# Performance work log

Hardware: AMD Instinct MI355X
Metric: run time of the kernel (lower is better)

## Reference

```python
import jax, jax.numpy as jnp
import numpy as np

EMB = 128  # embedding_size hard-coded in source
NW = 8192  # weak samples
NS = 8192  # strong samples
FD = 1024  # encoder input feature dim
QN = 1024  # queue max_size
C = 80     # num classes (COCO-style WSOD)


def setup_inputs() -> dict:
    key = jax.random.key(0)
    ks = jax.random.split(key, 9)
    return {
        "feats_strong": jax.random.normal(ks[0], (NS, FD), jnp.float32),
        "feats_weak": jax.random.normal(ks[1], (NW, FD), jnp.float32),
        "strong_labels": jax.random.randint(ks[2], (NS,), 0, C, jnp.int64),
        "weak_labels": jax.random.randint(ks[3], (NW,), 0, C, jnp.int64),
        "Wq": jax.random.normal(ks[4], (FD, EMB), jnp.float32) * (FD ** -0.5),
        "bq": jax.random.normal(ks[5], (EMB,), jnp.float32) * 0.01,
        "Wk": jax.random.normal(ks[6], (FD, EMB), jnp.float32) * (FD ** -0.5),
        "bk": jax.random.normal(ks[7], (EMB,), jnp.float32) * 0.01,
        "queue": jax.random.normal(ks[8], (QN, EMB), jnp.float32),
    }


def reference(feats_strong, feats_weak, strong_labels, weak_labels, Wq, bq, Wk, bk, queue):
    # Encoders applied to all samples at once (original loops one-by-one).
    q_all = feats_weak @ Wq + bq            # [NW, EMB]
    k_all = feats_strong @ Wk + bk          # [NS, EMB]
    k_all = jax.lax.stop_gradient(k_all)    # k = k.detach() in source

    w, s = weak_labels, strong_labels
    eq_ws = w[:, None] == s[None, :]                      # [NW, NS] weak-vs-strong label match
    cnt = eq_ws.astype(jnp.int32).sum(1)                  # num_strong per weak sample
    valid = cnt > 0                                       # `if weak_label in strong_labels`

    # rank of i among weak indices with the same label (position in torch.where output)
    eq_ww = (w[:, None] == w[None, :]).astype(jnp.int32)
    rank = jnp.tril(eq_ww, -1).sum(1)                     # [NW]
    sel = rank % jnp.maximum(cnt, 1)                      # `% num_strong`

    # occurrence rank of each strong index within its label group
    eq_ss = (s[:, None] == s[None, :]).astype(jnp.int32)
    occ = jnp.tril(eq_ss, -1).sum(1)                      # [NS]

    # index_strong[i] = sel[i]-th strong index whose label == w[i]
    M = eq_ws & (occ[None, :] == sel[:, None])            # [NW, NS]
    idx = jnp.argmax(M, axis=1)                           # [NW]

    q = q_all                                             # [NW, EMB]
    k = k_all[idx]                                        # [NW, EMB]

    l_pos = jnp.sum(q * k, axis=-1, keepdims=True)        # bmm([N,1,E],[N,E,1]) -> [N,1]
    l_neg = q @ queue.reshape(EMB, -1)                    # queue.view(EMB, -1): row-major reshape
    logits = jnp.concatenate([l_pos, l_neg], axis=1)      # [NW, 1+QN]

    # CrossEntropy with target 0 on each valid row, mean over valid rows
    ce = -jax.nn.log_softmax(logits, axis=-1)[:, 0]
    m = valid.astype(logits.dtype)
    loss = jnp.sum(ce * m) / jnp.maximum(m.sum(), 1.0)
    return loss
```

## Files before the change

kernel.cpp:

```cpp
#include <hip/hip_runtime.h>
#include <hip/hip_bf16.h>

#define NW   8192
#define NS   8192
#define FD   1024
#define EMB  128
#define QN   1024
#define NC   80

typedef unsigned short ushort_t;
typedef unsigned int   uint_t;
typedef __attribute__((ext_vector_type(8))) short short8;
typedef __attribute__((ext_vector_type(4))) float f32x4;

#define OFF_Q      0u
#define OFF_K      1048576u
#define OFF_WTQ    2097152u
#define OFF_WTK    2129920u
#define OFF_HIST   2752512u
#define OFF_RANK   2752640u
#define OFF_CNT    2760832u
#define OFF_BHS    2785408u
#define OFF_BHW    2787968u
#define OFF_ACC    2790528u
#define OFF_QT     2790532u
#define OFF_TABLE  3000000u

__device__ __forceinline__ ushort_t f2bf(float f) {
    uint_t u = __float_as_uint(f);
    u = (u + 0x7fffu + ((u >> 16) & 1u)) >> 16;
    return (ushort_t)u;
}
__device__ __forceinline__ uint_t pack2(float a, float b) {
    return (uint_t)f2bf(a) | ((uint_t)f2bf(b) << 16);
}

#define GLOAD_LDS16(gp, lp)                                                     \
    __builtin_amdgcn_global_load_lds(                                           \
        (const __attribute__((address_space(1))) void*)(gp),                    \
        (__attribute__((address_space(3))) void*)(lp), 16, 0, 0)

__global__ __launch_bounds__(256) void cvtbh_k(const float* __restrict__ Wq,
                                               const float* __restrict__ Wk,
                                               const float* __restrict__ queue,
                                               const int* __restrict__ s_lab,
                                               const int* __restrict__ w_lab,
                                               ushort_t* __restrict__ Wtq,
                                               ushort_t* __restrict__ Wtk,
                                               ushort_t* __restrict__ Qt,
                                               int* __restrict__ bhs,
                                               int* __restrict__ bhw,
                                               float* __restrict__ accum,
                                               int* __restrict__ counter) {
    int bx = blockIdx.x;
    int t = threadIdx.x;
    if (bx >= 384) {
        __shared__ int h[NC];
        int b2 = bx - 384, z = b2 >> 5, cb = b2 & 31;
        const int* lab = z ? w_lab : s_lab;
        int* bh = z ? bhw : bhs;
        if (t < NC) h[t] = 0;
        __syncthreads();
        atomicAdd(&h[lab[cb * 256 + t]], 1);
        __syncthreads();
        if (t < NC) bh[cb * NC + t] = h[t];
        return;
    }
    __shared__ float tile[32][33];
    int z = bx >> 7, flat = bx & 127;
    if (z == 0 && flat == 0) {
        if (t < 2) accum[t] = 0.0f;
        if (t == 2) *counter = 0;
    }
    const float* in; ushort_t* out; int r0, c0, C;
    if (z < 2) { in = z ? Wk : Wq; out = z ? Wtk : Wtq; C = 128;
                 r0 = (flat >> 2) * 32; c0 = (flat & 3) * 32; }
    else       { in = queue; out = Qt; C = 1024;
                 r0 = (flat & 3) * 32; c0 = (flat >> 2) * 32; }
    int i = t >> 3, j0 = (t & 7) * 4;
    float4 v = *(const float4*)(in + (size_t)(r0 + i) * C + c0 + j0);
    tile[i][j0] = v.x; tile[i][j0 + 1] = v.y; tile[i][j0 + 2] = v.z; tile[i][j0 + 3] = v.w;
    __syncthreads();
    uint2 pk;
    pk.x = pack2(tile[j0][i], tile[j0 + 1][i]);
    pk.y = pack2(tile[j0 + 2][i], tile[j0 + 3][i]);
    size_t oaddr;
    if (z < 2) {
        int k0 = r0 + j0, n = c0 + i;
        oaddr = (size_t)(k0 >> 5) * 4096 + (size_t)((k0 >> 3) & 3) * 1024
              + (size_t)n * 8 + (k0 & 7);
    } else {
        oaddr = (size_t)(c0 + i) * 128 + (r0 + j0);
    }
    *(uint2*)(out + oaddr) = pk;
}

__global__ __launch_bounds__(256) void enc_mfma_k(const float* __restrict__ A0,
                                                  const float* __restrict__ A1,
                                                  const ushort_t* __restrict__ Wt0,
                                                  const ushort_t* __restrict__ Wt1,
                                                  const float* __restrict__ b0_,
                                                  const float* __restrict__ b1_,
                                                  float* __restrict__ out0,
                                                  float* __restrict__ out1,
                                                  const int* __restrict__ s_lab,
                                                  const int* __restrict__ w_lab,
                                                  const int* __restrict__ bhs,
                                                  const int* __restrict__ bhw,
                                                  int* __restrict__ table,
                                                  int* __restrict__ rank,
                                                  int* __restrict__ hist) {
    __shared__ __align__(16) char smem[20480];

    int bx = blockIdx.x;
    int t = threadIdx.x;

    if (bx >= 1024) {
        int* ll = (int*)smem;
        int b2 = bx - 1024, z = b2 >> 5, cb = b2 & 31;
        const int* lab = z ? w_lab : s_lab;
        const int* bh = z ? bhw : bhs;
        int j = cb * 256 + t;
        int c = lab[j];
        ll[t] = c;
        __syncthreads();
        int r = 0;
        for (int b = 0; b < cb; b++) r += bh[b * NC + c];
        for (int jj = 0; jj < t; jj++) r += (ll[jj] == c) ? 1 : 0;
        if (z) rank[j] = r;
        else   table[c * 8192 + r] = j;
        if (b2 == 0 && t < 128) {
            int h = 0;
            if (t < NC)
                for (int b = 0; b < 32; b++) h += bhs[b * NC + t];
            hist[t] = h;
        }
        return;
    }

    int which = bx >> 9;
    int mtile = bx & 511;
    const float*    A    = which ? A1 : A0;
    const ushort_t* Wt   = which ? Wt1 : Wt0;
    const float*    bias = which ? b1_ : b0_;
    float*          out  = which ? out1 : out0;
    int row0 = mtile * 16;

    int wv = t >> 6, ln = t & 63;
    int lane15 = ln & 15, kg = ln >> 4;

    const float* gA = A + (size_t)(row0 + wv * 8 + (ln >> 3)) * FD + ((ln & 7) ^ (ln >> 3)) * 4;
    const ushort_t* gB = Wt + (size_t)wv * 1024 + ln * 8;

    f32x4 acc0 = (f32x4){0.f, 0.f, 0.f, 0.f};
    f32x4 acc1 = (f32x4){0.f, 0.f, 0.f, 0.f};

#define STAGE(BUF, KB)                                                           \
    { char* lb = smem + (BUF) * 10240;                                           \
      if (wv < 2) GLOAD_LDS16(gA + (size_t)(KB) * 32, lb + wv * 1024);           \
      const ushort_t* gb = gB + (size_t)(KB) * 4096;                             \
      char* bb = lb + 2048 + wv * 2048;                                          \
      GLOAD_LDS16(gb,       bb);                                                 \
      GLOAD_LDS16(gb + 512, bb + 1024); }

    STAGE(0, 0)
    __syncthreads();

#pragma unroll 1
    for (int kb = 0; kb < 32; kb++) {
        int cur = kb & 1;
        if (kb < 31) STAGE(cur ^ 1, kb + 1)
        char* lb = smem + cur * 10240;
        float4 alo = *(const float4*)(lb + (lane15 * 8 + ((2 * kg)     ^ (lane15 & 7))) * 16);
        float4 ahi = *(const float4*)(lb + (lane15 * 8 + ((2 * kg + 1) ^ (lane15 & 7))) * 16);
        uint4 pk;
        pk.x = pack2(alo.x, alo.y); pk.y = pack2(alo.z, alo.w);
        pk.z = pack2(ahi.x, ahi.y); pk.w = pack2(ahi.z, ahi.w);
        short8 af = __builtin_bit_cast(short8, pk);
        uint4 bb0 = *(const uint4*)(lb + 2048 + ((size_t)kg * 128 + wv * 32 + lane15) * 16);
        uint4 bb1 = *(const uint4*)(lb + 2048 + ((size_t)kg * 128 + wv * 32 + 16 + lane15) * 16);
        acc0 = __builtin_amdgcn_mfma_f32_16x16x32_bf16(af, __builtin_bit_cast(short8, bb0), acc0, 0, 0, 0);
        acc1 = __builtin_amdgcn_mfma_f32_16x16x32_bf16(af, __builtin_bit_cast(short8, bb1), acc1, 0, 0, 0);
        __syncthreads();
    }
#undef STAGE

    {
        int col0 = wv * 32 + lane15, col1 = wv * 32 + 16 + lane15;
        float bv0 = bias[col0], bv1 = bias[col1];
        int rbase = row0 + kg * 4;
#pragma unroll
        for (int j = 0; j < 4; j++) {
            out[(size_t)(rbase + j) * EMB + col0] = acc0[j] + bv0;
            out[(size_t)(rbase + j) * EMB + col1] = acc1[j] + bv1;
        }
    }
}

__global__ __launch_bounds__(256, 2) void ce_mfma_k(const float* __restrict__ q,
                                                    const float* __restrict__ k,
                                                    const ushort_t* __restrict__ Qt,
                                                    const int* __restrict__ rank,
                                                    const int* __restrict__ table,
                                                    const int* __restrict__ w,
                                                    const int* __restrict__ hist,
                                                    float* __restrict__ accum,
                                                    int* __restrict__ counter,
                                                    float* __restrict__ outp) {
    __shared__ int   idx_lds[16];
    __shared__ float lpos_lds[16];
    __shared__ float mg[4][16][2];
    int t = threadIdx.x;
    int r0 = blockIdx.x * 16;

    if (t < 16) {
        int i = r0 + t;
        int c = w[i];
        int cc = hist[c];
        idx_lds[t] = (cc > 0) ? table[c * 8192 + (rank[i] % cc)] : 0;
    }
    __syncthreads();

    {
        int rr = t >> 4;
        int o = (t & 15) * 8;
        const float4* qa = (const float4*)(q + (size_t)(r0 + rr) * EMB + o);
        const float4* ka = (const float4*)(k + (size_t)idx_lds[rr] * EMB + o);
        float4 a0 = qa[0], b0 = ka[0], a1 = qa[1], b1 = ka[1];
        float s = a0.x * b0.x + a0.y * b0.y + a0.z * b0.z + a0.w * b0.w
                + a1.x * b1.x + a1.y * b1.y + a1.z * b1.z + a1.w * b1.w;
        s += __shfl_xor(s, 1); s += __shfl_xor(s, 2);
        s += __shfl_xor(s, 4); s += __shfl_xor(s, 8);
        if ((t & 15) == 0) lpos_lds[rr] = s;
    }

    int wv = t >> 6, ln = t & 63;
    int lane15 = ln & 15, kg = ln >> 4;

    short8 afr[4];
#pragma unroll
    for (int ks = 0; ks < 4; ks++) {
        const float4* p = (const float4*)(q + (size_t)(r0 + lane15) * EMB + ks * 32 + kg * 8);
        float4 a = p[0], b = p[1];
        uint4 pk;
        pk.x = pack2(a.x, a.y); pk.y = pack2(a.z, a.w);
        pk.z = pack2(b.x, b.y); pk.w = pack2(b.z, b.w);
        afr[ks] = __builtin_bit_cast(short8, pk);
    }

    f32x4 accA[8], accB[8];
#pragma unroll
    for (int nc = 0; nc < 8; nc++) {
        accA[nc] = (f32x4){0.f, 0.f, 0.f, 0.f};
        accB[nc] = (f32x4){0.f, 0.f, 0.f, 0.f};
    }
#pragma unroll
    for (int nc = 0; nc < 8; nc++) {
        size_t nrow0 = (size_t)(nc * 128 + wv * 32 + lane15) * 128 + kg * 8;
#pragma unroll
        for (int ks = 0; ks < 4; ks++) {
            short8 bf0 = __builtin_bit_cast(short8, *(const uint4*)(Qt + nrow0 + ks * 32));
            short8 bf1 = __builtin_bit_cast(short8, *(const uint4*)(Qt + nrow0 + 16 * 128 + ks * 32));
            accA[nc] = __builtin_amdgcn_mfma_f32_16x16x32_bf16(afr[ks], bf0, accA[nc], 0, 0, 0);
            accB[nc] = __builtin_amdgcn_mfma_f32_16x16x32_bf16(afr[ks], bf1, accB[nc], 0, 0, 0);
        }
    }

#pragma unroll
    for (int j = 0; j < 4; j++) {
        float mx = -1e30f;
#pragma unroll
        for (int nc = 0; nc < 8; nc++) mx = fmaxf(mx, fmaxf(accA[nc][j], accB[nc][j]));
        mx = fmaxf(mx, __shfl_xor(mx, 1));
        mx = fmaxf(mx, __shfl_xor(mx, 2));
        mx = fmaxf(mx, __shfl_xor(mx, 4));
        mx = fmaxf(mx, __shfl_xor(mx, 8));
        float s = 0.f;
#pragma unroll
        for (int nc = 0; nc < 8; nc++)
            s += __expf(accA[nc][j] - mx) + __expf(accB[nc][j] - mx);
        s += __shfl_xor(s, 1);
        s += __shfl_xor(s, 2);
        s += __shfl_xor(s, 4);
        s += __shfl_xor(s, 8);
        if (lane15 == 0) {
            mg[wv][kg * 4 + j][0] = mx;
            mg[wv][kg * 4 + j][1] = s;
        }
    }
    __syncthreads();
    if (wv == 0) {
        float cv = 0.f, cc = 0.f;
        if (t < 16) {
            int i = r0 + t;
            float m0 = mg[0][t][0], l0 = mg[0][t][1];
            float m1 = mg[1][t][0], l1 = mg[1][t][1];
            float m2 = mg[2][t][0], l2 = mg[2][t][1];
            float m3 = mg[3][t][0], l3 = mg[3][t][1];
            float lp = lpos_lds[t];
            float m = fmaxf(fmaxf(fmaxf(m0, m1), fmaxf(m2, m3)), lp);
            float l = l0 * __expf(m0 - m) + l1 * __expf(m1 - m)
                    + l2 * __expf(m2 - m) + l3 * __expf(m3 - m) + __expf(lp - m);
            float ce = -(lp - m - __logf(l));
            if (hist[w[i]] > 0) { cv = ce; cc = 1.f; }
        }
        cv += __shfl_xor(cv, 1);  cc += __shfl_xor(cc, 1);
        cv += __shfl_xor(cv, 2);  cc += __shfl_xor(cc, 2);
        cv += __shfl_xor(cv, 4);  cc += __shfl_xor(cc, 4);
        cv += __shfl_xor(cv, 8);  cc += __shfl_xor(cc, 8);
        if (t == 0) {
            atomicAdd(&accum[0], cv);
            atomicAdd(&accum[1], cc);
            __threadfence();
            int done = atomicAdd(counter, 1);
            if (done == 511) {
                float s = atomicAdd(&accum[0], 0.0f);
                float c = atomicAdd(&accum[1], 0.0f);
                outp[0] = s / fmaxf(c, 1.0f);
            }
        }
    }
}

extern "C" void kernel_launch(void* const* d_in, const int* in_sizes, int n_in,
                              void* d_out, int out_size, void* d_ws, size_t ws_size,
                              hipStream_t stream) {
    const float* feats_strong = (const float*)d_in[0];
    const float* feats_weak   = (const float*)d_in[1];
    const int*   s_lab        = (const int*)d_in[2];
    const int*   w_lab        = (const int*)d_in[3];
    const float* Wq           = (const float*)d_in[4];
    const float* bq           = (const float*)d_in[5];
    const float* Wk           = (const float*)d_in[6];
    const float* bk           = (const float*)d_in[7];
    const float* queue        = (const float*)d_in[8];

    float*    wsf = (float*)d_ws;
    int*      wsi = (int*)d_ws;

    float*    q_g   = wsf + OFF_Q;
    float*    k_g   = wsf + OFF_K;
    int*      table = wsi + OFF_TABLE;
    ushort_t* Wtq   = (ushort_t*)(wsi + OFF_WTQ);
    ushort_t* Wtk   = (ushort_t*)(wsi + OFF_WTK);
    int*      hist  = wsi + OFF_HIST;
    int*      rank  = wsi + OFF_RANK;
    int*      cnt   = wsi + OFF_CNT;
    int*      bhs   = wsi + OFF_BHS;
    int*      bhw   = wsi + OFF_BHW;
    float*    accum = wsf + OFF_ACC;
    ushort_t* Qt    = (ushort_t*)(wsi + OFF_QT);

    cvtbh_k<<<448, 256, 0, stream>>>(Wq, Wk, queue, s_lab, w_lab,
                                     Wtq, Wtk, Qt, bhs, bhw, accum, cnt);
    enc_mfma_k<<<1088, 256, 0, stream>>>(feats_weak, feats_strong, Wtq, Wtk, bq, bk, q_g, k_g,
                                         s_lab, w_lab, bhs, bhw, table, rank, hist);
    ce_mfma_k<<<512, 256, 0, stream>>>(q_g, k_g, Qt, rank, table, w_lab, hist,
                                       accum, cnt, (float*)d_out);
}
```

Before: 170.2 us.

## Enlarge encoder GEMM tiles and stage queue through swizzled LDS in CE kernel

The encoder GEMM now computes 32-row tiles with a 2x2 wave layout over a 64-wide K step, so each wave issues four MFMAs per A fragment. This halves the grid and the number of K iterations, and raises reuse of B per byte loaded. The weight pre-layout changes to match the 64-wide K blocking. In the CE kernel, the transposed queue is laid out with an XOR swizzle and streamed through double-buffered LDS via global-to-LDS loads, replacing direct global fragment reads. The trade-off is more LDS per block (48KB encoder, 32KB CE), which may lower occupancy, plus an extra barrier per N chunk in the CE loop.

```diff
diff --git a/kernel.cpp b/kernel.cpp
--- a/kernel.cpp
+++ b/kernel.cpp
@@ -85,12 +85,13 @@
     pk.x = pack2(tile[j0][i], tile[j0 + 1][i]);
     pk.y = pack2(tile[j0 + 2][i], tile[j0 + 3][i]);
     size_t oaddr;
+    int k0 = r0 + j0, n = c0 + i;
     if (z < 2) {
-        int k0 = r0 + j0, n = c0 + i;
-        oaddr = (size_t)(k0 >> 5) * 4096 + (size_t)((k0 >> 3) & 3) * 1024
+        oaddr = (size_t)(k0 >> 6) * 8192 + (size_t)((k0 >> 3) & 7) * 1024
               + (size_t)n * 8 + (k0 & 7);
     } else {
-        oaddr = (size_t)(c0 + i) * 128 + (r0 + j0);
+        int c = k0 >> 3;
+        oaddr = ((size_t)n * 16 + (c ^ (n & 15))) * 8 + (k0 & 7);
     }
     *(uint2*)(out + oaddr) = pk;
 }
@@ -110,14 +111,14 @@
                                                   int* __restrict__ table,
                                                   int* __restrict__ rank,
                                                   int* __restrict__ hist) {
-    __shared__ __align__(16) char smem[20480];
+    __shared__ __align__(16) char smem[49152];
 
     int bx = blockIdx.x;
     int t = threadIdx.x;
 
-    if (bx >= 1024) {
+    if (bx >= 512) {
         int* ll = (int*)smem;
-        int b2 = bx - 1024, z = b2 >> 5, cb = b2 & 31;
+        int b2 = bx - 512, z = b2 >> 5, cb = b2 & 31;
         const int* lab = z ? w_lab : s_lab;
         const int* bh = z ? bhw : bhs;
         int j = cb * 256 + t;
@@ -138,62 +139,78 @@
         return;
     }
 
-    int which = bx >> 9;
-    int mtile = bx & 511;
+    int which = bx >> 8;
+    int mtile = bx & 255;
     const float*    A    = which ? A1 : A0;
     const ushort_t* Wt   = which ? Wt1 : Wt0;
     const float*    bias = which ? b1_ : b0_;
     float*          out  = which ? out1 : out0;
-    int row0 = mtile * 16;
+    int row0 = mtile * 32;
 
     int wv = t >> 6, ln = t & 63;
+    int wm = wv >> 1, wn = wv & 1;
     int lane15 = ln & 15, kg = ln >> 4;
 
-    const float* gA = A + (size_t)(row0 + wv * 8 + (ln >> 3)) * FD + ((ln & 7) ^ (ln >> 3)) * 4;
-    const ushort_t* gB = Wt + (size_t)wv * 1024 + ln * 8;
-
-    f32x4 acc0 = (f32x4){0.f, 0.f, 0.f, 0.f};
-    f32x4 acc1 = (f32x4){0.f, 0.f, 0.f, 0.f};
+    int ar0 = wv * 8 + (ln >> 4);
+    int ar1 = ar0 + 4;
+    const float* gA0 = A + (size_t)(row0 + ar0) * FD + (((ln & 15) ^ (ar0 & 15))) * 4;
+    const float* gA1 = A + (size_t)(row0 + ar1) * FD + (((ln & 15) ^ (ar1 & 15))) * 4;
+    const ushort_t* gB = Wt + (size_t)wv * 2048 + ln * 8;
+
+    f32x4 acc[4];
+#pragma unroll
+    for (int nt = 0; nt < 4; nt++) acc[nt] = (f32x4){0.f, 0.f, 0.f, 0.f};
 
 #define STAGE(BUF, KB)                                                           \
-    { char* lb = smem + (BUF) * 10240;                                           \
-      if (wv < 2) GLOAD_LDS16(gA + (size_t)(KB) * 32, lb + wv * 1024);           \
-      const ushort_t* gb = gB + (size_t)(KB) * 4096;                             \
-      char* bb = lb + 2048 + wv * 2048;                                          \
-      GLOAD_LDS16(gb,       bb);                                                 \
-      GLOAD_LDS16(gb + 512, bb + 1024); }
+    { char* lb = smem + (BUF) * 24576;                                           \
+      GLOAD_LDS16(gA0 + (size_t)(KB) * 64, lb + wv * 2048);                      \
+      GLOAD_LDS16(gA1 + (size_t)(KB) * 64, lb + wv * 2048 + 1024);               \
+      const ushort_t* gb = gB + (size_t)(KB) * 8192;                             \
+      char* bb = lb + 8192 + wv * 4096;                                          \
+      GLOAD_LDS16(gb,        bb);                                                \
+      GLOAD_LDS16(gb + 512,  bb + 1024);                                         \
+      GLOAD_LDS16(gb + 1024, bb + 2048);                                         \
+      GLOAD_LDS16(gb + 1536, bb + 3072); }
 
     STAGE(0, 0)
     __syncthreads();
 
 #pragma unroll 1
-    for (int kb = 0; kb < 32; kb++) {
+    for (int kb = 0; kb < 16; kb++) {
         int cur = kb & 1;
-        if (kb < 31) STAGE(cur ^ 1, kb + 1)
-        char* lb = smem + cur * 10240;
-        float4 alo = *(const float4*)(lb + (lane15 * 8 + ((2 * kg)     ^ (lane15 & 7))) * 16);
-        float4 ahi = *(const float4*)(lb + (lane15 * 8 + ((2 * kg + 1) ^ (lane15 & 7))) * 16);
-        uint4 pk;
-        pk.x = pack2(alo.x, alo.y); pk.y = pack2(alo.z, alo.w);
-        pk.z = pack2(ahi.x, ahi.y); pk.w = pack2(ahi.z, ahi.w);
-        short8 af = __builtin_bit_cast(short8, pk);
-        uint4 bb0 = *(const uint4*)(lb + 2048 + ((size_t)kg * 128 + wv * 32 + lane15) * 16);
-        uint4 bb1 = *(const uint4*)(lb + 2048 + ((size_t)kg * 128 + wv * 32 + 16 + lane15) * 16);
-        acc0 = __builtin_amdgcn_mfma_f32_16x16x32_bf16(af, __builtin_bit_cast(short8, bb0), acc0, 0, 0, 0);
-        acc1 = __builtin_amdgcn_mfma_f32_16x16x32_bf16(af, __builtin_bit_cast(short8, bb1), acc1, 0, 0, 0);
+        if (kb < 15) STAGE(cur ^ 1, kb + 1)
+        char* lb = smem + cur * 24576;
+#pragma unroll
+        for (int ks = 0; ks < 2; ks++) {
+            int r_l = wm * 16 + lane15;
+            int c0 = ks * 8 + kg * 2;
+            float4 alo = *(const float4*)(lb + ((size_t)r_l * 16 + ((c0)     ^ (r_l & 15))) * 16);
+            float4 ahi = *(const float4*)(lb + ((size_t)r_l * 16 + ((c0 + 1) ^ (r_l & 15))) * 16);
+            uint4 pk;
+            pk.x = pack2(alo.x, alo.y); pk.y = pack2(alo.z, alo.w);
+            pk.z = pack2(ahi.x, ahi.y); pk.w = pack2(ahi.z, ahi.w);
+            short8 af = __builtin_bit_cast(short8, pk);
+            int kgg = ks * 4 + kg;
+#pragma unroll
+            for (int nt = 0; nt < 4; nt++) {
+                uint4 bb = *(const uint4*)(lb + 8192 +
+                            ((size_t)kgg * 128 + wn * 64 + nt * 16 + lane15) * 16);
+                acc[nt] = __builtin_amdgcn_mfma_f32_16x16x32_bf16(
+                    af, __builtin_bit_cast(short8, bb), acc[nt], 0, 0, 0);
+            }
+        }
         __syncthreads();
     }
 #undef STAGE
 
-    {
-        int col0 = wv * 32 + lane15, col1 = wv * 32 + 16 + lane15;
-        float bv0 = bias[col0], bv1 = bias[col1];
-        int rbase = row0 + kg * 4;
-#pragma unroll
-        for (int j = 0; j < 4; j++) {
-            out[(size_t)(rbase + j) * EMB + col0] = acc0[j] + bv0;
-            out[(size_t)(rbase + j) * EMB + col1] = acc1[j] + bv1;
-        }
+#pragma unroll
+    for (int nt = 0; nt < 4; nt++) {
+        int col = wn * 64 + nt * 16 + lane15;
+        float bv = bias[col];
+        int rbase = row0 + wm * 16 + kg * 4;
+#pragma unroll
+        for (int j = 0; j < 4; j++)
+            out[(size_t)(rbase + j) * EMB + col] = acc[nt][j] + bv;
     }
 }
 
@@ -207,6 +224,7 @@
                                                     float* __restrict__ accum,
                                                     int* __restrict__ counter,
                                                     float* __restrict__ outp) {
+    __shared__ __align__(16) char bsm[32768];
     __shared__ int   idx_lds[16];
     __shared__ float lpos_lds[16];
     __shared__ float mg[4][16][2];
@@ -248,37 +266,51 @@
         afr[ks] = __builtin_bit_cast(short8, pk);
     }
 
-    f32x4 accA[8], accB[8];
-#pragma unroll
-    for (int nc = 0; nc < 8; nc++) {
-        accA[nc] = (f32x4){0.f, 0.f, 0.f, 0.f};
-        accB[nc] = (f32x4){0.f, 0.f, 0.f, 0.f};
-    }
-#pragma unroll
-    for (int nc = 0; nc < 8; nc++) {
-        size_t nrow0 = (size_t)(nc * 128 + wv * 32 + lane15) * 128 + kg * 8;
+    f32x4 acc[16];
+#pragma unroll
+    for (int nc = 0; nc < 16; nc++) acc[nc] = (f32x4){0.f, 0.f, 0.f, 0.f};
+
+#define STAGE_CE(BUF, NC)                                                        \
+    { char* lb = bsm + (BUF) * 16384;                                            \
+      const ushort_t* src = Qt + (size_t)(NC) * 8192 + wv * 2048 + ln * 8;       \
+      char* bb = lb + wv * 4096;                                                 \
+      GLOAD_LDS16(src,        bb);                                               \
+      GLOAD_LDS16(src + 512,  bb + 1024);                                        \
+      GLOAD_LDS16(src + 1024, bb + 2048);                                        \
+      GLOAD_LDS16(src + 1536, bb + 3072); }
+
+    STAGE_CE(0, 0)
+    __syncthreads();
+
+#pragma unroll
+    for (int nc = 0; nc < 16; nc++) {
+        int cur = nc & 1;
+        if (nc < 15) STAGE_CE(cur ^ 1, nc + 1)
+        char* lb = bsm + cur * 16384;
+        int n_l = wv * 16 + lane15;
 #pragma unroll
         for (int ks = 0; ks < 4; ks++) {
-            short8 bf0 = __builtin_bit_cast(short8, *(const uint4*)(Qt + nrow0 + ks * 32));
-            short8 bf1 = __builtin_bit_cast(short8, *(const uint4*)(Qt + nrow0 + 16 * 128 + ks * 32));
-            accA[nc] = __builtin_amdgcn_mfma_f32_16x16x32_bf16(afr[ks], bf0, accA[nc], 0, 0, 0);
-            accB[nc] = __builtin_amdgcn_mfma_f32_16x16x32_bf16(afr[ks], bf1, accB[nc], 0, 0, 0);
-        }
-    }
+            int c = ks * 4 + kg;
+            uint4 bb = *(const uint4*)(lb + ((size_t)n_l * 16 + (c ^ lane15)) * 16);
+            acc[nc] = __builtin_amdgcn_mfma_f32_16x16x32_bf16(
+                afr[ks], __builtin_bit_cast(short8, bb), acc[nc], 0, 0, 0);
+        }
+        __syncthreads();
+    }
+#undef STAGE_CE
 
 #pragma unroll
     for (int j = 0; j < 4; j++) {
         float mx = -1e30f;
 #pragma unroll
-        for (int nc = 0; nc < 8; nc++) mx = fmaxf(mx, fmaxf(accA[nc][j], accB[nc][j]));
+        for (int nc = 0; nc < 16; nc++) mx = fmaxf(mx, acc[nc][j]);
         mx = fmaxf(mx, __shfl_xor(mx, 1));
         mx = fmaxf(mx, __shfl_xor(mx, 2));
         mx = fmaxf(mx, __shfl_xor(mx, 4));
         mx = fmaxf(mx, __shfl_xor(mx, 8));
         float s = 0.f;
 #pragma unroll
-        for (int nc = 0; nc < 8; nc++)
-            s += __expf(accA[nc][j] - mx) + __expf(accB[nc][j] - mx);
+        for (int nc = 0; nc < 16; nc++) s += __expf(acc[nc][j] - mx);
         s += __shfl_xor(s, 1);
         s += __shfl_xor(s, 2);
         s += __shfl_xor(s, 4);
@@ -353,8 +385,8 @@
 
     cvtbh_k<<<448, 256, 0, stream>>>(Wq, Wk, queue, s_lab, w_lab,
                                      Wtq, Wtk, Qt, bhs, bhw, accum, cnt);
-    enc_mfma_k<<<1088, 256, 0, stream>>>(feats_weak, feats_strong, Wtq, Wtk, bq, bk, q_g, k_g,
-                                         s_lab, w_lab, bhs, bhw, table, rank, hist);
+    enc_mfma_k<<<576, 256, 0, stream>>>(feats_weak, feats_strong, Wtq, Wtk, bq, bk, q_g, k_g,
+                                        s_lab, w_lab, bhs, bhw, table, rank, hist);
     ce_mfma_k<<<512, 256, 0, stream>>>(q_g, k_g, Qt, rank, table, w_lab, hist,
                                        accum, cnt, (float*)d_out);
 }
```

After: 154.5 us. 1.1x faster.
